# Kernel optimization log

Measured on AMD Instinct MI355X. Metric: run time of the kernel, lower is better.

The kernel has to match this reference:

```python
import jax, jax.numpy as jnp
import numpy as np

BETA = 0.9        # LIF membrane decay
THRESHOLD = 1.0   # LIF firing threshold
SURROGATE_K = 25.0  # superspike surrogate slope (spyx default)

@jax.custom_vjp
def spike(u):
    return (u > 0.0).astype(u.dtype)

def _spike_fwd(u):
    return spike(u), u

def _spike_bwd(u, g):
    # superspike surrogate gradient
    return (g / (1.0 + SURROGATE_K * jnp.abs(u)) ** 2,)

spike.defvjp(_spike_fwd, _spike_bwd)

def lif(V, I):
    # leaky integrate, fire, reset-by-subtraction (spyx snn.LIF semantics)
    V = BETA * V + I
    s = spike(V - THRESHOLD)
    V = V - s * THRESHOLD
    return s, V

def setup_inputs() -> dict:
    key = jax.random.key(0)
    ks = jax.random.split(key, 9)
    T, B, D, H, L = 512, 64, 1024, 2048, 256
    def lin(k, fan_in, shape):
        return jax.random.normal(k, shape, jnp.float32) / np.sqrt(fan_in)
    return {
        "x_seq": jax.random.normal(ks[0], (T, B, D), jnp.float32),
        "W_enc": lin(ks[1], D, (D, H)), "b_enc": jnp.zeros((H,), jnp.float32),
        "W_lat": lin(ks[2], H, (H, L)), "b_lat": jnp.zeros((L,), jnp.float32),
        "W_dec": lin(ks[3], L, (L, H)), "b_dec": jnp.zeros((H,), jnp.float32),
        "W_rec": lin(ks[4], H, (H, D)), "b_rec": jnp.zeros((D,), jnp.float32),
    }

def reference(x_seq, W_enc, b_enc, W_lat, b_lat, W_dec, b_dec, W_rec, b_rec):
    T, B, D = x_seq.shape
    H, L = W_enc.shape[1], W_lat.shape[1]
    V0 = (jnp.zeros((B, H), x_seq.dtype),
          jnp.zeros((B, L), x_seq.dtype),
          jnp.zeros((B, H), x_seq.dtype))

    def step(carry, x_t):
        Ve, Vl, Vd = carry
        s_enc, Ve = lif(Ve, x_t @ W_enc + b_enc)      # [B,H]
        z_t, Vl = lif(Vl, s_enc @ W_lat + b_lat)      # [B,L]
        s_dec, Vd = lif(Vd, z_t @ W_dec + b_dec)      # [B,H]
        recon_t = s_dec @ W_rec + b_rec               # [B,D]
        sr_t = jnp.stack([jnp.mean(s_enc), jnp.mean(z_t), jnp.mean(s_dec)])
        return (Ve, Vl, Vd), (recon_t, z_t, sr_t)

    _, (recon_seq, latent_seq, sr_seq) = jax.lax.scan(step, V0, x_seq)
    recon = jnp.mean(recon_seq, axis=0)  # readout='mean'
    spike_rate = jnp.mean(sr_seq, axis=0)
    recon_err = jnp.mean(jnp.abs(recon_seq - x_seq))
    return recon, recon_seq, latent_seq, spike_rate, recon_err
```

## Files before the change

kernel.cpp:

```cpp
#include <hip/hip_runtime.h>


#define T_STEPS 512
#define BB 64
#define DD 1024
#define HH 2048
#define LL 256
#define KC_PANEL 512

template<typename AT>
__global__ __launch_bounds__(256) void gemm_panel(
    const AT* __restrict__ A, const float* __restrict__ Bm,
    const float* __restrict__ bias, float* __restrict__ C,
    int M, int N, int K)
{
  __shared__ float As[16][128];
  __shared__ float Bs[16][64];
  const int tid = threadIdx.x;
  const int tx = tid & 15, ty = tid >> 4;
  const int row0 = blockIdx.y * 128, col0 = blockIdx.x * 64;
  const int ar = tid >> 1;
  const int ak = (tid & 1) * 8;
  const int br = tid >> 4;
  const int bn = (tid & 15) * 4;

  float acc[8][4] = {};
  float pacc[8][4] = {};
  const int KT = K >> 4;
  for (int kt = 0; kt < KT; ++kt) {
    if (kt > 0 && ((kt * 16) % KC_PANEL) == 0) {
      #pragma unroll
      for (int i = 0; i < 8; ++i)
        #pragma unroll
        for (int j = 0; j < 4; ++j) {
          acc[i][j] = __fadd_rn(acc[i][j], pacc[i][j]);
          pacc[i][j] = 0.0f;
        }
    }
    float a[8];
    if constexpr (sizeof(AT) == 1) {
      unsigned long long w =
          *(const unsigned long long*)(A + (size_t)(row0 + ar) * K + kt * 16 + ak);
      #pragma unroll
      for (int j = 0; j < 8; ++j) a[j] = (float)((w >> (8 * j)) & 0xFFull);
    } else {
      const float* ap = (const float*)A + (size_t)(row0 + ar) * K + kt * 16 + ak;
      float4 f0 = *(const float4*)ap;
      float4 f1 = *(const float4*)(ap + 4);
      a[0] = f0.x; a[1] = f0.y; a[2] = f0.z; a[3] = f0.w;
      a[4] = f1.x; a[5] = f1.y; a[6] = f1.z; a[7] = f1.w;
    }
    float4 bf = *(const float4*)(Bm + (size_t)(kt * 16 + br) * N + col0 + bn);
    __syncthreads();
    #pragma unroll
    for (int j = 0; j < 8; ++j) As[ak + j][ar] = a[j];
    Bs[br][bn + 0] = bf.x; Bs[br][bn + 1] = bf.y;
    Bs[br][bn + 2] = bf.z; Bs[br][bn + 3] = bf.w;
    __syncthreads();
    #pragma unroll
    for (int k = 0; k < 16; ++k) {
      float av[8], bv[4];
      #pragma unroll
      for (int i = 0; i < 8; ++i) av[i] = As[k][ty * 8 + i];
      #pragma unroll
      for (int j = 0; j < 4; ++j) bv[j] = Bs[k][tx * 4 + j];
      #pragma unroll
      for (int i = 0; i < 8; ++i)
        #pragma unroll
        for (int j = 0; j < 4; ++j)
          pacc[i][j] = fmaf(av[i], bv[j], pacc[i][j]);
    }
  }
  #pragma unroll
  for (int i = 0; i < 8; ++i)
    #pragma unroll
    for (int j = 0; j < 4; ++j) {
      float tot = __fadd_rn(acc[i][j], pacc[i][j]);
      tot = __fadd_rn(tot, bias[col0 + tx * 4 + j]);
      C[(size_t)(row0 + ty * 8 + i) * N + col0 + tx * 4 + j] = tot;
    }
}

__global__ __launch_bounds__(256) void lif_scan(
    const float* __restrict__ I, float* __restrict__ V,
    unsigned char* __restrict__ S, float* __restrict__ latent,
    unsigned long long* __restrict__ cnt, int Tc, int NTOT)
{
  const int idx = blockIdx.x * 256 + threadIdx.x;
  float v = V[idx];
  unsigned c = 0;
  for (int t = 0; t < Tc; ++t) {
    v = fmaf(0.9f, v, I[(size_t)t * NTOT + idx]);
    const bool s = __fsub_rn(v, 1.0f) > 0.0f;
    if (s) v = __fsub_rn(v, 1.0f);
    S[(size_t)t * NTOT + idx] = (unsigned char)s;
    if (latent) latent[(size_t)t * NTOT + idx] = s ? 1.0f : 0.0f;
    c += (unsigned)s;
  }
  V[idx] = v;
  unsigned long long cc = c;
  for (int o = 32; o; o >>= 1) cc += __shfl_down(cc, o);
  if ((threadIdx.x & 63) == 0 && cc) atomicAdd(cnt, cc);
}

__global__ __launch_bounds__(256) void recon_mean_kernel(
    const float* __restrict__ rs, float* __restrict__ out)
{
  const int idx = blockIdx.x * 256 + threadIdx.x;
  double s = 0.0;
  for (int t = 0; t < T_STEPS; ++t) s += (double)rs[(size_t)t * 65536 + idx];
  out[idx] = (float)(s * (1.0 / 512.0));
}

__global__ __launch_bounds__(256) void err_kernel(
    const float* __restrict__ rs, const float* __restrict__ x,
    double* __restrict__ acc)
{
  const size_t N = (size_t)T_STEPS * BB * DD;
  double s = 0.0;
  for (size_t i = (size_t)blockIdx.x * 256 + threadIdx.x; i < N;
       i += (size_t)gridDim.x * 256)
    s += (double)fabsf(rs[i] - x[i]);
  for (int o = 32; o; o >>= 1) s += __shfl_down(s, o);
  __shared__ double wsum[4];
  if ((threadIdx.x & 63) == 0) wsum[threadIdx.x >> 6] = s;
  __syncthreads();
  if (threadIdx.x == 0) atomicAdd(acc, wsum[0] + wsum[1] + wsum[2] + wsum[3]);
}

__global__ void finalize_kernel(const double* __restrict__ acc,
                                const unsigned long long* __restrict__ cnt,
                                float* __restrict__ sr, float* __restrict__ err)
{
  if (threadIdx.x == 0) {
    sr[0] = (float)((double)cnt[0] / (512.0 * 64.0 * 2048.0));
    sr[1] = (float)((double)cnt[1] / (512.0 * 64.0 * 256.0));
    sr[2] = (float)((double)cnt[2] / (512.0 * 64.0 * 2048.0));
    err[0] = (float)(acc[0] / (512.0 * 64.0 * 1024.0));
  }
}

extern "C" void kernel_launch(void* const* d_in, const int* in_sizes, int n_in,
                              void* d_out, int out_size, void* d_ws, size_t ws_size,
                              hipStream_t stream) {
  const float* x    = (const float*)d_in[0];
  const float* Wenc = (const float*)d_in[1];
  const float* benc = (const float*)d_in[2];
  const float* Wlat = (const float*)d_in[3];
  const float* blat = (const float*)d_in[4];
  const float* Wdec = (const float*)d_in[5];
  const float* bdec = (const float*)d_in[6];
  const float* Wrec = (const float*)d_in[7];
  const float* brec = (const float*)d_in[8];

  float* out = (float*)d_out;
  float* recon     = out;
  float* recon_seq = out + 65536;
  float* latent    = recon_seq + (size_t)T_STEPS * BB * DD;
  float* sr        = latent + (size_t)T_STEPS * BB * LL;
  float* errp      = sr + 3;

  char* ws = (char*)d_ws;
  float* Ve = (float*)ws;
  float* Vl = (float*)(ws + 524288);
  float* Vd = (float*)(ws + 589824);
  unsigned long long* cnt = (unsigned long long*)(ws + 1114112);
  double* errAcc = (double*)(ws + 1114136);
  const size_t STATE = 1114368;

  unsigned char* Senc = (unsigned char*)(ws + STATE);
  unsigned char* Sdec = Senc;
  const size_t Z_OFF    = STATE + 67108864;
  unsigned char* Z      = (unsigned char*)(ws + Z_OFF);
  const size_t ILAT_OFF = Z_OFF + 8388608;
  float* Ilat           = (float*)(ws + ILAT_OFF);
  const size_t ICH_OFF  = ILAT_OFF + 33554432;
  float* Ichunk         = (float*)(ws + ICH_OFF);

  int Tc = 512;
  while (Tc > 2 && ICH_OFF + (size_t)Tc * 524288 > ws_size) Tc >>= 1;

  hipMemsetAsync(ws, 0, STATE, stream);

  for (int c0 = 0; c0 < T_STEPS; c0 += Tc) {
    gemm_panel<float><<<dim3(HH / 64, Tc * BB / 128), 256, 0, stream>>>(
        x + (size_t)c0 * BB * DD, Wenc, benc, Ichunk, Tc * BB, HH, DD);
    lif_scan<<<512, 256, 0, stream>>>(
        Ichunk, Ve, Senc + (size_t)c0 * BB * HH, nullptr, &cnt[0], Tc, BB * HH);
  }
  gemm_panel<unsigned char><<<dim3(LL / 64, T_STEPS * BB / 128), 256, 0, stream>>>(
      Senc, Wlat, blat, Ilat, T_STEPS * BB, LL, HH);
  lif_scan<<<64, 256, 0, stream>>>(
      Ilat, Vl, Z, latent, &cnt[1], T_STEPS, BB * LL);
  for (int c0 = 0; c0 < T_STEPS; c0 += Tc) {
    gemm_panel<unsigned char><<<dim3(HH / 64, Tc * BB / 128), 256, 0, stream>>>(
        Z + (size_t)c0 * BB * LL, Wdec, bdec, Ichunk, Tc * BB, HH, LL);
    lif_scan<<<512, 256, 0, stream>>>(
        Ichunk, Vd, Sdec + (size_t)c0 * BB * HH, nullptr, &cnt[2], Tc, BB * HH);
    gemm_panel<unsigned char><<<dim3(DD / 64, Tc * BB / 128), 256, 0, stream>>>(
        Sdec + (size_t)c0 * BB * HH, Wrec, brec,
        recon_seq + (size_t)c0 * BB * DD, Tc * BB, DD, HH);
  }

  recon_mean_kernel<<<256, 256, 0, stream>>>(recon_seq, recon);
  err_kernel<<<2048, 256, 0, stream>>>(recon_seq, x, errAcc);
  finalize_kernel<<<1, 64, 0, stream>>>(errAcc, cnt, sr, errp);
}
```

Measured before the change: 4.605 ms.

## Enlarge GEMM tile to 128x128 with double-buffered shared memory and vector loads

The panel GEMM goes from 128x64 tiles with a 16-deep k-step to 128x128 tiles with an 8-deep k-step. Each thread now holds an 8x8 accumulator, and the shared-memory buffers are double-buffered so the next tile's global fetch overlaps the current compute with one barrier per step. LDS reads and output stores become float4 vector accesses. The partial-sum flush interval stays at 512 in k, so the rounding order is kept. The cost is higher register pressure from 128 accumulator floats per thread and half as many blocks, which may lower occupancy on the narrow L=256 GEMM.

Result: slower. 4.788 ms (+4.0%).

```diff
diff --git a/kernel.cpp b/kernel.cpp
--- a/kernel.cpp
+++ b/kernel.cpp
@@ -6,7 +6,6 @@
 #define DD 1024
 #define HH 2048
 #define LL 256
-#define KC_PANEL 512
 
 template<typename AT>
 __global__ __launch_bounds__(256) void gemm_panel(
@@ -14,71 +13,88 @@
     const float* __restrict__ bias, float* __restrict__ C,
     int M, int N, int K)
 {
-  __shared__ float As[16][128];
-  __shared__ float Bs[16][64];
+  __shared__ float As[2][8][128];
+  __shared__ float Bs[2][8][128];
   const int tid = threadIdx.x;
   const int tx = tid & 15, ty = tid >> 4;
-  const int row0 = blockIdx.y * 128, col0 = blockIdx.x * 64;
-  const int ar = tid >> 1;
-  const int ak = (tid & 1) * 8;
-  const int br = tid >> 4;
-  const int bn = (tid & 15) * 4;
-
-  float acc[8][4] = {};
-  float pacc[8][4] = {};
-  const int KT = K >> 4;
+  const int row0 = blockIdx.y * 128, col0 = blockIdx.x * 128;
+  const int lar = tid >> 1;
+  const int lak = (tid & 1) * 4;
+  const int lbk = tid >> 5;
+  const int lbn = (tid & 31) * 4;
+
+  float acc[8][8] = {};
+  float pacc[8][8] = {};
+  const int KT = K >> 3;
+
+  float a4[4];
+  float4 b4;
+  auto fetch = [&](int kt) {
+    if constexpr (sizeof(AT) == 1) {
+      uchar4 u = *(const uchar4*)(A + (size_t)(row0 + lar) * K + kt * 8 + lak);
+      a4[0] = u.x; a4[1] = u.y; a4[2] = u.z; a4[3] = u.w;
+    } else {
+      float4 f = *(const float4*)((const float*)A + (size_t)(row0 + lar) * K + kt * 8 + lak);
+      a4[0] = f.x; a4[1] = f.y; a4[2] = f.z; a4[3] = f.w;
+    }
+    b4 = *(const float4*)(Bm + (size_t)(kt * 8 + lbk) * N + col0 + lbn);
+  };
+
+  fetch(0);
+  As[0][lak + 0][lar] = a4[0]; As[0][lak + 1][lar] = a4[1];
+  As[0][lak + 2][lar] = a4[2]; As[0][lak + 3][lar] = a4[3];
+  *(float4*)&Bs[0][lbk][lbn] = b4;
+  __syncthreads();
+
   for (int kt = 0; kt < KT; ++kt) {
-    if (kt > 0 && ((kt * 16) % KC_PANEL) == 0) {
+    const int cur = kt & 1;
+    if (kt > 0 && (kt & 63) == 0) {
       #pragma unroll
       for (int i = 0; i < 8; ++i)
         #pragma unroll
-        for (int j = 0; j < 4; ++j) {
+        for (int j = 0; j < 8; ++j) {
           acc[i][j] = __fadd_rn(acc[i][j], pacc[i][j]);
           pacc[i][j] = 0.0f;
         }
     }
-    float a[8];
-    if constexpr (sizeof(AT) == 1) {
-      unsigned long long w =
-          *(const unsigned long long*)(A + (size_t)(row0 + ar) * K + kt * 16 + ak);
-      #pragma unroll
-      for (int j = 0; j < 8; ++j) a[j] = (float)((w >> (8 * j)) & 0xFFull);
-    } else {
-      const float* ap = (const float*)A + (size_t)(row0 + ar) * K + kt * 16 + ak;
-      float4 f0 = *(const float4*)ap;
-      float4 f1 = *(const float4*)(ap + 4);
-      a[0] = f0.x; a[1] = f0.y; a[2] = f0.z; a[3] = f0.w;
-      a[4] = f1.x; a[5] = f1.y; a[6] = f1.z; a[7] = f1.w;
-    }
-    float4 bf = *(const float4*)(Bm + (size_t)(kt * 16 + br) * N + col0 + bn);
-    __syncthreads();
+    if (kt + 1 < KT) {
+      fetch(kt + 1);
+      const int nxt = cur ^ 1;
+      As[nxt][lak + 0][lar] = a4[0]; As[nxt][lak + 1][lar] = a4[1];
+      As[nxt][lak + 2][lar] = a4[2]; As[nxt][lak + 3][lar] = a4[3];
+      *(float4*)&Bs[nxt][lbk][lbn] = b4;
+    }
     #pragma unroll
-    for (int j = 0; j < 8; ++j) As[ak + j][ar] = a[j];
-    Bs[br][bn + 0] = bf.x; Bs[br][bn + 1] = bf.y;
-    Bs[br][bn + 2] = bf.z; Bs[br][bn + 3] = bf.w;
-    __syncthreads();
-    #pragma unroll
-    for (int k = 0; k < 16; ++k) {
-      float av[8], bv[4];
-      #pragma unroll
-      for (int i = 0; i < 8; ++i) av[i] = As[k][ty * 8 + i];
-      #pragma unroll
-      for (int j = 0; j < 4; ++j) bv[j] = Bs[k][tx * 4 + j];
+    for (int k = 0; k < 8; ++k) {
+      float av[8], bv[8];
+      *(float4*)&av[0] = *(const float4*)&As[cur][k][ty * 8];
+      *(float4*)&av[4] = *(const float4*)&As[cur][k][ty * 8 + 4];
+      *(float4*)&bv[0] = *(const float4*)&Bs[cur][k][tx * 8];
+      *(float4*)&bv[4] = *(const float4*)&Bs[cur][k][tx * 8 + 4];
       #pragma unroll
       for (int i = 0; i < 8; ++i)
         #pragma unroll
-        for (int j = 0; j < 4; ++j)
+        for (int j = 0; j < 8; ++j)
           pacc[i][j] = fmaf(av[i], bv[j], pacc[i][j]);
     }
-  }
+    __syncthreads();
+  }
+
   #pragma unroll
-  for (int i = 0; i < 8; ++i)
+  for (int i = 0; i < 8; ++i) {
+    float bb[8];
+    *(float4*)&bb[0] = *(const float4*)&bias[col0 + tx * 8];
+    *(float4*)&bb[4] = *(const float4*)&bias[col0 + tx * 8 + 4];
+    float o[8];
     #pragma unroll
-    for (int j = 0; j < 4; ++j) {
+    for (int j = 0; j < 8; ++j) {
       float tot = __fadd_rn(acc[i][j], pacc[i][j]);
-      tot = __fadd_rn(tot, bias[col0 + tx * 4 + j]);
-      C[(size_t)(row0 + ty * 8 + i) * N + col0 + tx * 4 + j] = tot;
-    }
+      o[j] = __fadd_rn(tot, bb[j]);
+    }
+    const size_t r = (size_t)(row0 + ty * 8 + i) * N + col0 + tx * 8;
+    *(float4*)&C[r] = *(const float4*)&o[0];
+    *(float4*)&C[r + 4] = *(const float4*)&o[4];
+  }
 }
 
 __global__ __launch_bounds__(256) void lif_scan(
@@ -183,21 +199,21 @@
   hipMemsetAsync(ws, 0, STATE, stream);
 
   for (int c0 = 0; c0 < T_STEPS; c0 += Tc) {
-    gemm_panel<float><<<dim3(HH / 64, Tc * BB / 128), 256, 0, stream>>>(
+    gemm_panel<float><<<dim3(HH / 128, Tc * BB / 128), 256, 0, stream>>>(
         x + (size_t)c0 * BB * DD, Wenc, benc, Ichunk, Tc * BB, HH, DD);
     lif_scan<<<512, 256, 0, stream>>>(
         Ichunk, Ve, Senc + (size_t)c0 * BB * HH, nullptr, &cnt[0], Tc, BB * HH);
   }
-  gemm_panel<unsigned char><<<dim3(LL / 64, T_STEPS * BB / 128), 256, 0, stream>>>(
+  gemm_panel<unsigned char><<<dim3(LL / 128, T_STEPS * BB / 128), 256, 0, stream>>>(
       Senc, Wlat, blat, Ilat, T_STEPS * BB, LL, HH);
   lif_scan<<<64, 256, 0, stream>>>(
       Ilat, Vl, Z, latent, &cnt[1], T_STEPS, BB * LL);
   for (int c0 = 0; c0 < T_STEPS; c0 += Tc) {
-    gemm_panel<unsigned char><<<dim3(HH / 64, Tc * BB / 128), 256, 0, stream>>>(
+    gemm_panel<unsigned char><<<dim3(HH / 128, Tc * BB / 128), 256, 0, stream>>>(
         Z + (size_t)c0 * BB * LL, Wdec, bdec, Ichunk, Tc * BB, HH, LL);
     lif_scan<<<512, 256, 0, stream>>>(
         Ichunk, Vd, Sdec + (size_t)c0 * BB * HH, nullptr, &cnt[2], Tc, BB * HH);
-    gemm_panel<unsigned char><<<dim3(DD / 64, Tc * BB / 128), 256, 0, stream>>>(
+    gemm_panel<unsigned char><<<dim3(DD / 128, Tc * BB / 128), 256, 0, stream>>>(
         Sdec + (size_t)c0 * BB * HH, Wrec, brec,
         recon_seq + (size_t)c0 * BB * DD, Tc * BB, DD, HH);
   }
```
